# Kernel optimization log

Hardware: AMD Instinct MI355X
Metric: run time of the kernel (lower is better)

The kernel has to match this reference:

```python
import jax, jax.numpy as jnp
import numpy as np

VOCAB_SIZE = 256  # matches init kwarg vocab_size
NUM_WORDS = 262144
WORD_LEN = 32


def setup_inputs() -> dict:
    key = jax.random.key(0)
    k1, = jax.random.split(key, 1)
    x = jax.random.randint(k1, (NUM_WORDS, WORD_LEN), 0, VOCAB_SIZE, dtype=jnp.int64)
    # learned scalar forgetting factor (nn.Parameter init 0.0 in source; use 0.9 for
    # numerically non-degenerate testing -- math is identical)
    forgetting_factor = jnp.float32(0.9)
    return {"x": x, "forgetting_factor": forgetting_factor}


def reference(x, forgetting_factor):
    # Original recurrence per word: for each char c_k with c_k != 0:
    #   z = f * z + onehot(c_k);  chars equal to 0 are skipped entirely (no decay).
    # Closed form: z = sum_k [c_k != 0] * f^(#nonzero chars strictly after k) * onehot(c_k)
    mask_i = (x != 0).astype(jnp.int32)                      # [W, L]
    # nonzero chars strictly after position k (reverse cumsum minus self)
    s = jnp.cumsum(mask_i[:, ::-1], axis=1)[:, ::-1] - mask_i  # [W, L] int
    sf = s.astype(jnp.float32)
    # safe power: avoid nan grads of f**0; exponent clamped then where'd back to 1.0
    w = jnp.power(forgetting_factor, jnp.maximum(sf, 1.0))
    w = jnp.where(s == 0, jnp.float32(1.0), w) * mask_i.astype(jnp.float32)  # [W, L]
    num_words = x.shape[0]
    rows = jnp.arange(num_words)[:, None]                    # [W, 1]
    out = jnp.zeros((num_words, VOCAB_SIZE), dtype=jnp.float32)
    out = out.at[rows, x].add(w)                             # weighted one-hot scatter-sum
    return out
```

## Files before the change

### kernel.cpp

```cpp
#include <hip/hip_runtime.h>


constexpr int WORD_LEN = 32;
constexpr int VOCAB    = 256;
constexpr int WAVES_PER_BLOCK = 4;
constexpr int WORDS_PER_WAVE  = 16;

typedef float f32x4 __attribute__((ext_vector_type(4)));
typedef int   i32x2 __attribute__((ext_vector_type(2)));

__global__ __launch_bounds__(256) void fofe_kernel(
    const int* __restrict__ x,
    const float* __restrict__ fptr,
    float* __restrict__ out,
    int num_words)
{
    __shared__ float tiles[WAVES_PER_BLOCK][4][VOCAB];

    const int lane = threadIdx.x & 63;
    const int wv   = threadIdx.x >> 6;
    const int grp  = lane >> 4;
    const int j    = lane & 15;

    const int gw = blockIdx.x * WAVES_PER_BLOCK + wv;
    const int w0 = gw * WORDS_PER_WAVE;

    const i32x2* x2 = reinterpret_cast<const i32x2*>(x);

    i32x2 c[4];
#pragma unroll
    for (int q = 0; q < 4; ++q) {
        c[q] = (i32x2)(0);
        if (w0 + 4 * q + grp < num_words)
            c[q] = x2[(size_t)(w0 + 4 * q) * 16 + lane];
    }

    const float f  = *fptr;
    const float lf = __log2f(f);

    float (*mytiles)[VOCAB] = tiles[wv];
    float*  tile = mytiles[grp];
    f32x4*  t4   = reinterpret_cast<f32x4*>(mytiles);

#pragma unroll
    for (int q = 0; q < 4; ++q) {
        const int wq = w0 + 4 * q;
        const i32x2 cc = c[q];

        const bool nzE = (cc.x != 0);
        const bool nzO = (cc.y != 0);
        const unsigned long long mE = __ballot(nzE);
        const unsigned long long mO = __ballot(nzO);
        const unsigned int mEg = (unsigned int)(mE >> (grp * 16)) & 0xFFFFu;
        const unsigned int mOg = (unsigned int)(mO >> (grp * 16)) & 0xFFFFu;
        const int sE = __popc(mEg >> (j + 1)) + __popc(mOg >> j);
        const int sO = __popc(mEg >> (j + 1)) + __popc(mOg >> (j + 1));

        float wE = 0.0f, wO = 0.0f;
        if (nzE) wE = (sE == 0) ? 1.0f : exp2f((float)sE * lf);
        if (nzO) wO = (sO == 0) ? 1.0f : exp2f((float)sO * lf);

        const f32x4 z = (f32x4)(0.0f);
        t4[lane]       = z;
        t4[lane + 64]  = z;
        t4[lane + 128] = z;
        t4[lane + 192] = z;

        if (nzE) atomicAdd(&tile[cc.x], wE);
        if (nzO) atomicAdd(&tile[cc.y], wO);

        const f32x4 v0 = t4[lane];
        const f32x4 v1 = t4[lane + 64];
        const f32x4 v2 = t4[lane + 128];
        const f32x4 v3 = t4[lane + 192];
        f32x4* o4 = reinterpret_cast<f32x4*>(out + (size_t)wq * VOCAB);
        if (wq + 0 < num_words) __builtin_nontemporal_store(v0, &o4[lane]);
        if (wq + 1 < num_words) __builtin_nontemporal_store(v1, &o4[lane + 64]);
        if (wq + 2 < num_words) __builtin_nontemporal_store(v2, &o4[lane + 128]);
        if (wq + 3 < num_words) __builtin_nontemporal_store(v3, &o4[lane + 192]);
    }
}

extern "C" void kernel_launch(void* const* d_in, const int* in_sizes, int n_in,
                              void* d_out, int out_size, void* d_ws, size_t ws_size,
                              hipStream_t stream)
{
    const int*   x    = (const int*)d_in[0];
    const float* fptr = (const float*)d_in[1];
    float*       out  = (float*)d_out;

    const int num_words = in_sizes[0] / WORD_LEN;
    const int waves  = (num_words + WORDS_PER_WAVE - 1) / WORDS_PER_WAVE;
    const int blocks = (waves + WAVES_PER_BLOCK - 1) / WAVES_PER_BLOCK;

    fofe_kernel<<<blocks, 256, 0, stream>>>(x, fptr, out, num_words);
}
```

Before: 57.44 us.

## Convert to persistent grid-stride kernel with two-deep load prefetch

Replaces the one-shot grid (each wave handling 16 words) with a fixed grid of 512 blocks. Each wave strides over 4-word quads and keeps loads two iterations ahead in registers, so input reads overlap with the LDS scatter and the output stores. This cuts block launch overhead and aims to hide load latency, at the cost of lower occupancy and a loop-carried dependency.

```diff
diff --git a/kernel.cpp b/kernel.cpp
--- a/kernel.cpp
+++ b/kernel.cpp
@@ -4,7 +4,7 @@
 constexpr int WORD_LEN = 32;
 constexpr int VOCAB    = 256;
 constexpr int WAVES_PER_BLOCK = 4;
-constexpr int WORDS_PER_WAVE  = 16;
+constexpr int NUM_BLOCKS      = 512;
 
 typedef float f32x4 __attribute__((ext_vector_type(4)));
 typedef int   i32x2 __attribute__((ext_vector_type(2)));
@@ -23,17 +23,10 @@
     const int j    = lane & 15;
 
     const int gw = blockIdx.x * WAVES_PER_BLOCK + wv;
-    const int w0 = gw * WORDS_PER_WAVE;
+    const int nw = NUM_BLOCKS * WAVES_PER_BLOCK;
+    const int nquads = (num_words + 3) >> 2;
 
     const i32x2* x2 = reinterpret_cast<const i32x2*>(x);
-
-    i32x2 c[4];
-#pragma unroll
-    for (int q = 0; q < 4; ++q) {
-        c[q] = (i32x2)(0);
-        if (w0 + 4 * q + grp < num_words)
-            c[q] = x2[(size_t)(w0 + 4 * q) * 16 + lane];
-    }
 
     const float f  = *fptr;
     const float lf = __log2f(f);
@@ -42,11 +35,14 @@
     float*  tile = mytiles[grp];
     f32x4*  t4   = reinterpret_cast<f32x4*>(mytiles);
 
-#pragma unroll
-    for (int q = 0; q < 4; ++q) {
-        const int wq = w0 + 4 * q;
-        const i32x2 cc = c[q];
+    auto load_quad = [&](int q) -> i32x2 {
+        i32x2 c = (i32x2)(0);
+        if (q < nquads && q * 4 + grp < num_words)
+            c = x2[(size_t)q * 64 + lane];
+        return c;
+    };
 
+    auto process = [&](int wq, i32x2 cc) {
         const bool nzE = (cc.x != 0);
         const bool nzO = (cc.y != 0);
         const unsigned long long mE = __ballot(nzE);
@@ -78,6 +74,16 @@
         if (wq + 1 < num_words) __builtin_nontemporal_store(v1, &o4[lane + 64]);
         if (wq + 2 < num_words) __builtin_nontemporal_store(v2, &o4[lane + 128]);
         if (wq + 3 < num_words) __builtin_nontemporal_store(v3, &o4[lane + 192]);
+    };
+
+    i32x2 c0 = load_quad(gw);
+    i32x2 c1 = load_quad(gw + nw);
+
+    for (int q = gw; q < nquads; q += nw) {
+        i32x2 cp = load_quad(q + 2 * nw);
+        process(q * 4, c0);
+        c0 = c1;
+        c1 = cp;
     }
 }
 
@@ -90,8 +96,6 @@
     float*       out  = (float*)d_out;
 
     const int num_words = in_sizes[0] / WORD_LEN;
-    const int waves  = (num_words + WORDS_PER_WAVE - 1) / WORDS_PER_WAVE;
-    const int blocks = (waves + WAVES_PER_BLOCK - 1) / WAVES_PER_BLOCK;
 
-    fofe_kernel<<<blocks, 256, 0, stream>>>(x, fptr, out, num_words);
+    fofe_kernel<<<NUM_BLOCKS, 256, 0, stream>>>(x, fptr, out, num_words);
 }
```

Measured after the change: 59.23 us. +3.1%, slower.
